# Performance work log

Hardware: AMD Instinct MI355X
Metric: run time of the kernel (lower is better)

The kernel has to match this reference:

```python
import jax, jax.numpy as jnp
import numpy as np

EMBD_DIM = 512
HIDDEN_DIM = 512
TARGET_DIM = 128
BATCH = 64
MAX_SET = 2048


def setup_inputs() -> dict:
    key = jax.random.key(0)
    ks = jax.random.split(key, 10)
    E, H, T = EMBD_DIM, HIDDEN_DIM, TARGET_DIM
    s = lambda fan_in: 1.0 / np.sqrt(fan_in)
    return {
        "words": jax.random.normal(ks[0], (BATCH, MAX_SET, E), dtype=jnp.float32),
        # attention_layer: Linear(2E -> H) followed by tanh; v: (H, 1)
        "W_att": jax.random.uniform(ks[1], (2 * E, H), jnp.float32, -s(2 * E), s(2 * E)),
        "b_att": jax.random.uniform(ks[2], (H,), jnp.float32, -s(2 * E), s(2 * E)),
        "v": jax.random.normal(ks[3], (H, 1), dtype=jnp.float32),
        # pred_net: Linear(E,H) -> ReLU -> Linear(H,H) -> ReLU -> Linear(H,T)
        "W1": jax.random.uniform(ks[4], (E, H), jnp.float32, -s(E), s(E)),
        "b1": jax.random.uniform(ks[5], (H,), jnp.float32, -s(E), s(E)),
        "W2": jax.random.uniform(ks[6], (H, H), jnp.float32, -s(H), s(H)),
        "b2": jax.random.uniform(ks[7], (H,), jnp.float32, -s(H), s(H)),
        "W3": jax.random.uniform(ks[8], (H, T), jnp.float32, -s(H), s(H)),
        "b3": jax.random.uniform(ks[9], (T,), jnp.float32, -s(H), s(H)),
    }


def reference(words, W_att, b_att, v, W1, b1, W2, b2, W3, b3):
    # words: [B, S, E]. A row is "valid" iff its feature-sum is nonzero
    # (matches words.sum(2).abs().sign() in the torch code).
    mask = jnp.sign(jnp.abs(words.sum(-1)))           # [B, S], 0/1 float
    lengths = mask.sum(axis=1, keepdims=True)          # [B, 1]
    # context = mean over valid rows (padded rows are exactly zero)
    context = words.sum(axis=1, keepdims=True) / lengths[..., None]  # [B, 1, E]
    context = jnp.broadcast_to(context, words.shape)   # [B, S, E]

    x = jnp.concatenate([words, context], axis=-1)     # [B, S, 2E]
    h = jnp.tanh(x @ W_att + b_att)                    # [B, S, H]
    scores = (h @ v)[..., 0]                           # [B, S]

    # per-segment softmax over valid rows only (masked_select + per-batch
    # Softmax in the original == masked softmax here)
    scores = jnp.where(mask > 0, scores, jnp.full_like(scores, -1e30))
    attn = jax.nn.softmax(scores, axis=1)              # [B, S]

    rep = jnp.einsum("bs,bse->be", attn, words)        # [B, E]

    pred = jax.nn.relu(rep @ W1 + b1)
    pred = jax.nn.relu(pred @ W2 + b2)
    pred = pred @ W3 + b3                              # [B, T]
    return pred
```

## Files before the change

kernel.cpp:

```cpp
#include <hip/hip_runtime.h>
#include <hip/hip_bf16.h>
#include <hip/hip_fp16.h>
#include <math.h>

#define B 64
#define S 2048
#define E 512
#define HD 512
#define TD 128
#define M_TOT (B*S)

#define OFF_MASK   0
#define OFF_CTXP   (OFF_MASK + B*S)
#define OFF_LENP   (OFF_CTXP + 8*B*E)
#define OFF_CB     (OFF_LENP + 8*B)
#define OFF_REPP   (OFF_CB + B*HD)
#define OFF_SC     (OFF_REPP + 8*B*E)
#define OFF_WPK    (OFF_SC + B*S)

typedef __attribute__((ext_vector_type(8))) short short8;
typedef __attribute__((ext_vector_type(4))) float f32x4;

__device__ inline unsigned int f2hu(float x) {
    __half h = __float2half(x);
    unsigned short u; __builtin_memcpy(&u, &h, 2); return (unsigned int)u;
}

__device__ inline float fast_tanh(float x) {
    float a = fabsf(x);
    float e = __expf(-2.0f * a);
    float r = (1.0f - e) / (1.0f + e);
    return copysignf(r, x);
}

__global__ __launch_bounds__(256)
void k0_pack(const float* __restrict__ W_att, unsigned short* __restrict__ Wpk)
{
    int tid = blockIdx.x*256 + threadIdx.x;
    int e = tid >> 9, h = tid & 511;
    float w = W_att[(size_t)e*HD + h];
    int kstep = e >> 5, kb = (e >> 3) & 3, j = e & 7, f = h >> 4, l15 = h & 15;
    size_t dst = ((((size_t)kstep*32 + f)*64) + kb*16 + l15)*8 + j;
    Wpk[dst] = (unsigned short)f2hu(w);
}

__global__ __launch_bounds__(256)
void k1_maskcol(const float* __restrict__ words, float* __restrict__ mask,
                float* __restrict__ ctxp, float* __restrict__ lenp)
{
    int bid = blockIdx.x;
    int b = bid >> 3, ch = bid & 7;
    int t = threadIdx.x;
    int w = t >> 6, l = t & 63;
    __shared__ __align__(16) float colred[4][E];
    __shared__ float lenred[4];
    const float* base = words + (size_t)(b * S + ch * 256) * E;
    float4 c0 = make_float4(0.f,0.f,0.f,0.f), c1 = make_float4(0.f,0.f,0.f,0.f);
    float wlen = 0.0f;
    for (int r = w; r < 256; r += 4) {
        const float* row = base + (size_t)r * E;
        float4 a  = *(const float4*)(row + 4*l);
        float4 bb = *(const float4*)(row + 256 + 4*l);
        float rs = a.x+a.y+a.z+a.w + bb.x+bb.y+bb.z+bb.w;
        #pragma unroll
        for (int m = 1; m < 64; m <<= 1) rs += __shfl_xor(rs, m);
        c0.x += a.x;  c0.y += a.y;  c0.z += a.z;  c0.w += a.w;
        c1.x += bb.x; c1.y += bb.y; c1.z += bb.z; c1.w += bb.w;
        if (l == 0) {
            float mv = (rs != 0.0f) ? 1.0f : 0.0f;
            mask[(size_t)b*S + ch*256 + r] = mv;
            wlen += mv;
        }
    }
    *(float4*)&colred[w][4*l]       = c0;
    *(float4*)&colred[w][256 + 4*l] = c1;
    if (l == 0) lenred[w] = wlen;
    __syncthreads();
    float s1 = colred[0][t]+colred[1][t]+colred[2][t]+colred[3][t];
    float s2 = colred[0][t+256]+colred[1][t+256]+colred[2][t+256]+colred[3][t+256];
    size_t o = ((size_t)ch * B + b) * E;
    ctxp[o + t]       = s1;
    ctxp[o + t + 256] = s2;
    if (t == 0) lenp[ch*B + b] = lenred[0]+lenred[1]+lenred[2]+lenred[3];
}

__global__ __launch_bounds__(256)
void k2_cb(const float* __restrict__ W_att, const float* __restrict__ b_att,
           const float* __restrict__ ctxp, const float* __restrict__ lenp,
           float* __restrict__ cb)
{
    int bid = blockIdx.x;
    int b = bid >> 1, hc = bid & 1;
    int t = threadIdx.x;
    __shared__ float ctxL[E];
    float len = 0.f;
    #pragma unroll
    for (int k = 0; k < 8; ++k) len += lenp[k*B + b];
    float inv = 1.0f / len;
    for (int c = t; c < E; c += 256) {
        float sv = 0.f;
        #pragma unroll
        for (int k = 0; k < 8; ++k) sv += ctxp[((size_t)k*B + b)*E + c];
        ctxL[c] = sv * inv;
    }
    __syncthreads();
    int h = hc*256 + t;
    const float* Wb = W_att + (size_t)E * HD;
    float a0 = b_att[h], a1 = 0.f, a2 = 0.f, a3 = 0.f;
    #pragma unroll 4
    for (int e = 0; e < E; e += 4) {
        a0 += ctxL[e]   * Wb[(size_t)e*HD + h];
        a1 += ctxL[e+1] * Wb[(size_t)(e+1)*HD + h];
        a2 += ctxL[e+2] * Wb[(size_t)(e+2)*HD + h];
        a3 += ctxL[e+3] * Wb[(size_t)(e+3)*HD + h];
    }
    cb[(size_t)b*HD + h] = (a0 + a1) + (a2 + a3);
}

__global__ __launch_bounds__(512, 2)
void k3_scores(const float* __restrict__ words,
               const unsigned short* __restrict__ Wpk,
               const float* __restrict__ cb, const float* __restrict__ v,
               float* __restrict__ sc)
{
    __shared__ __align__(16) unsigned char smem[16384];
    int mt = blockIdx.x;
    int m0 = mt * 128;
    int b  = m0 >> 11;
    int t = threadIdx.x;
    int lane = t & 63, wid = t >> 6;
    int wr = wid >> 2, wc = wid & 3;

    f32x4 acc[4][8];
    #pragma unroll
    for (int i = 0; i < 4; ++i)
        #pragma unroll
        for (int j = 0; j < 8; ++j) acc[i][j] = (f32x4)0.0f;

    int sF = (t >> 6) & 7, skb = (t >> 4) & 3, sl15 = t & 15;
    int srow = sF*16 + sl15;
    const float* aSrc = words + (size_t)(m0 + srow)*E + skb*8;

    const unsigned short* bBase = Wpk + (((size_t)(wc*8))*64 + lane)*8;
#define LDB(kst,cf) (*(const short8*)(bBase + ((size_t)(kst)*32 + (cf))*512))

    float4 pa0, pa1, qa0, qa1;
#define LOADA(P0, P1, s) do { const float* _s = aSrc + (s)*32; \
        P0 = *(const float4*)(_s); P1 = *(const float4*)(_s + 4); } while(0)
#define STAGEA(buf, P0, P1) do { \
        unsigned int u0 = f2hu(P0.x) | (f2hu(P0.y) << 16); \
        unsigned int u1 = f2hu(P0.z) | (f2hu(P0.w) << 16); \
        unsigned int u2 = f2hu(P1.x) | (f2hu(P1.y) << 16); \
        unsigned int u3 = f2hu(P1.z) | (f2hu(P1.w) << 16); \
        *(uint4*)&(buf)[t*16] = make_uint4(u0, u1, u2, u3); } while(0)

    unsigned char* sm0 = smem;
    unsigned char* sm1 = smem + 8192;

    short8 bA[8], bB[8];

    LOADA(pa0, pa1, 0);
    STAGEA(sm0, pa0, pa1);
    LOADA(pa0, pa1, 1);
    LOADA(qa0, qa1, 2);
    #pragma unroll
    for (int cf = 0; cf < 8; ++cf) bA[cf] = LDB(0, cf);
    __syncthreads();

#define KBODY(k, BUFC, BUFN, P0, P1, BCUR, BNEXT) do { \
        short8 ah[4]; \
        _Pragma("unroll") \
        for (int rf = 0; rf < 4; ++rf) \
            ah[rf] = *(const short8*)&(BUFC)[(wr*4 + rf)*1024 + lane*16]; \
        if ((k) < 15) { \
            _Pragma("unroll") \
            for (int cf = 0; cf < 8; ++cf) BNEXT[cf] = LDB((k)+1, cf); \
            STAGEA(BUFN, P0, P1); \
        } \
        if ((k) < 13) LOADA(P0, P1, (k) + 3); \
        _Pragma("unroll") \
        for (int cf = 0; cf < 8; ++cf) { \
            _Pragma("unroll") \
            for (int rf = 0; rf < 4; ++rf) \
                acc[rf][cf] = __builtin_amdgcn_mfma_f32_16x16x32_f16(ah[rf], BCUR[cf], acc[rf][cf], 0, 0, 0); \
        } \
        __syncthreads(); } while(0)

    KBODY( 0, sm0, sm1, pa0, pa1, bA, bB);
    KBODY( 1, sm1, sm0, qa0, qa1, bB, bA);
    KBODY( 2, sm0, sm1, pa0, pa1, bA, bB);
    KBODY( 3, sm1, sm0, qa0, qa1, bB, bA);
    KBODY( 4, sm0, sm1, pa0, pa1, bA, bB);
    KBODY( 5, sm1, sm0, qa0, qa1, bB, bA);
    KBODY( 6, sm0, sm1, pa0, pa1, bA, bB);
    KBODY( 7, sm1, sm0, qa0, qa1, bB, bA);
    KBODY( 8, sm0, sm1, pa0, pa1, bA, bB);
    KBODY( 9, sm1, sm0, qa0, qa1, bB, bA);
    KBODY(10, sm0, sm1, pa0, pa1, bA, bB);
    KBODY(11, sm1, sm0, qa0, qa1, bB, bA);
    KBODY(12, sm0, sm1, pa0, pa1, bA, bB);
    KBODY(13, sm1, sm0, qa0, qa1, bB, bA);
    KBODY(14, sm0, sm1, pa0, pa1, bA, bB);
    KBODY(15, sm1, sm0, qa0, qa1, bB, bA);
#undef KBODY
#undef LOADA
#undef STAGEA
#undef LDB

    float ssum[4][4];
    #pragma unroll
    for (int i = 0; i < 4; ++i)
        #pragma unroll
        for (int rr = 0; rr < 4; ++rr) ssum[i][rr] = 0.f;

    #pragma unroll
    for (int cf = 0; cf < 8; ++cf) {
        int col = wc*128 + cf*16 + (lane & 15);
        float cbv = cb[(size_t)b*HD + col];
        float vv  = v[col];
        #pragma unroll
        for (int rf = 0; rf < 4; ++rf)
            #pragma unroll
            for (int rr = 0; rr < 4; ++rr)
                ssum[rf][rr] += fast_tanh(acc[rf][cf][rr] + cbv) * vv;
    }
    #pragma unroll
    for (int m = 1; m < 16; m <<= 1)
        #pragma unroll
        for (int rf = 0; rf < 4; ++rf)
            #pragma unroll
            for (int rr = 0; rr < 4; ++rr)
                ssum[rf][rr] += __shfl_xor(ssum[rf][rr], m);

    float* scr = (float*)smem;
    if ((lane & 15) == 0) {
        #pragma unroll
        for (int rf = 0; rf < 4; ++rf)
            #pragma unroll
            for (int rr = 0; rr < 4; ++rr)
                scr[wc*128 + wr*64 + rf*16 + (lane >> 4)*4 + rr] = ssum[rf][rr];
    }
    __syncthreads();
    if (t < 128) {
        float val = (scr[t] + scr[128 + t]) + (scr[256 + t] + scr[384 + t]);
        sc[(size_t)m0 + t] = val;
    }
}

__global__ __launch_bounds__(256)
void k4_rep(const float* __restrict__ words, const float* __restrict__ sc,
            const float* __restrict__ mask, float* __restrict__ repp)
{
    int bid = blockIdx.x;
    int b = bid >> 3, ch = bid & 7;
    int t = threadIdx.x;
    __shared__ float red[256];
    __shared__ float wrow[256];

    float xs[8];
    float mx = -1e30f;
    #pragma unroll
    for (int k = 0; k < 8; ++k) {
        size_t m = (size_t)b*S + 256*k + t;
        float x = sc[m];
        x = (mask[m] > 0.0f) ? x : -1e30f;
        xs[k] = x; mx = fmaxf(mx, x);
    }
    red[t] = mx; __syncthreads();
    for (int off = 128; off > 0; off >>= 1) {
        if (t < off) red[t] = fmaxf(red[t], red[t+off]);
        __syncthreads();
    }
    float gmax = red[0]; __syncthreads();
    float se = 0.f;
    #pragma unroll
    for (int k = 0; k < 8; ++k) se += expf(xs[k] - gmax);
    red[t] = se; __syncthreads();
    for (int off = 128; off > 0; off >>= 1) {
        if (t < off) red[t] += red[t+off];
        __syncthreads();
    }
    float den = red[0];
    wrow[t] = expf(xs[ch] - gmax) / den;
    __syncthreads();

    const float* base = words + (size_t)(b*S + ch*256)*E + 2*t;
    float2 acc = make_float2(0.f, 0.f);
    #pragma unroll 4
    for (int rr = 0; rr < 256; ++rr) {
        float2 wv = *(const float2*)(base + (size_t)rr*E);
        float a = wrow[rr];
        acc.x = fmaf(a, wv.x, acc.x);
        acc.y = fmaf(a, wv.y, acc.y);
    }
    size_t o = ((size_t)ch*B + b)*E + 2*t;
    *(float2*)&repp[o] = acc;
}

__global__ __launch_bounds__(256)
void k5_mlp(const float* __restrict__ repp,
            const float* __restrict__ W1, const float* __restrict__ b1,
            const float* __restrict__ W2, const float* __restrict__ b2,
            const float* __restrict__ W3, const float* __restrict__ b3,
            float* __restrict__ out)
{
    int b = blockIdx.x;
    int t = threadIdx.x;
    __shared__ float xL[HD];
    __shared__ float yL[HD];
    for (int c = t; c < E; c += 256) {
        float sv = 0.f;
        #pragma unroll
        for (int k = 0; k < 8; ++k) sv += repp[((size_t)k*B + b)*E + c];
        xL[c] = sv;
    }
    __syncthreads();
    #pragma unroll
    for (int oo = 0; oo < 2; ++oo) {
        int h = oo*256 + t;
        float a0 = b1[h], a1 = 0.f, a2 = 0.f, a3 = 0.f;
        #pragma unroll 4
        for (int e = 0; e < E; e += 4) {
            a0 += xL[e]   * W1[(size_t)e*HD + h];
            a1 += xL[e+1] * W1[(size_t)(e+1)*HD + h];
            a2 += xL[e+2] * W1[(size_t)(e+2)*HD + h];
            a3 += xL[e+3] * W1[(size_t)(e+3)*HD + h];
        }
        yL[h] = fmaxf((a0 + a1) + (a2 + a3), 0.f);
    }
    __syncthreads();
    float l2v[2];
    #pragma unroll
    for (int oo = 0; oo < 2; ++oo) {
        int h = oo*256 + t;
        float a0 = b2[h], a1 = 0.f, a2 = 0.f, a3 = 0.f;
        #pragma unroll 4
        for (int e = 0; e < HD; e += 4) {
            a0 += yL[e]   * W2[(size_t)e*HD + h];
            a1 += yL[e+1] * W2[(size_t)(e+1)*HD + h];
            a2 += yL[e+2] * W2[(size_t)(e+2)*HD + h];
            a3 += yL[e+3] * W2[(size_t)(e+3)*HD + h];
        }
        l2v[oo] = fmaxf((a0 + a1) + (a2 + a3), 0.f);
    }
    __syncthreads();
    xL[t] = l2v[0]; xL[256 + t] = l2v[1];
    __syncthreads();
    if (t < TD) {
        float a0 = b3[t], a1 = 0.f, a2 = 0.f, a3 = 0.f;
        #pragma unroll 4
        for (int e = 0; e < HD; e += 4) {
            a0 += xL[e]   * W3[(size_t)e*TD + t];
            a1 += xL[e+1] * W3[(size_t)(e+1)*TD + t];
            a2 += xL[e+2] * W3[(size_t)(e+2)*TD + t];
            a3 += xL[e+3] * W3[(size_t)(e+3)*TD + t];
        }
        out[(size_t)b*TD + t] = (a0 + a1) + (a2 + a3);
    }
}

extern "C" void kernel_launch(void* const* d_in, const int* in_sizes, int n_in,
                              void* d_out, int out_size, void* d_ws, size_t ws_size,
                              hipStream_t stream)
{
    const float* words = (const float*)d_in[0];
    const float* W_att = (const float*)d_in[1];
    const float* b_att = (const float*)d_in[2];
    const float* v     = (const float*)d_in[3];
    const float* W1    = (const float*)d_in[4];
    const float* b1    = (const float*)d_in[5];
    const float* W2    = (const float*)d_in[6];
    const float* b2    = (const float*)d_in[7];
    const float* W3    = (const float*)d_in[8];
    const float* b3    = (const float*)d_in[9];
    (void)in_sizes; (void)n_in; (void)out_size; (void)ws_size;

    float* ws   = (float*)d_ws;
    float* mask = ws + OFF_MASK;
    float* ctxp = ws + OFF_CTXP;
    float* lenp = ws + OFF_LENP;
    float* cb   = ws + OFF_CB;
    float* repp = ws + OFF_REPP;
    float* sc   = ws + OFF_SC;
    unsigned short* Wpk = (unsigned short*)(ws + OFF_WPK);
    float* out  = (float*)d_out;

    hipLaunchKernelGGL(k0_pack,    dim3(1024), dim3(256), 0, stream, W_att, Wpk);
    hipLaunchKernelGGL(k1_maskcol, dim3(B*8),  dim3(256), 0, stream, words, mask, ctxp, lenp);
    hipLaunchKernelGGL(k2_cb,      dim3(B*2),  dim3(256), 0, stream, W_att, b_att, ctxp, lenp, cb);
    hipLaunchKernelGGL(k3_scores,  dim3(1024), dim3(512), 0, stream, words, Wpk, cb, v, sc);
    hipLaunchKernelGGL(k4_rep,     dim3(B*8),  dim3(256), 0, stream, words, sc, mask, repp);
    hipLaunchKernelGGL(k5_mlp,     dim3(B),    dim3(256), 0, stream, repp, W1, b1, W2, b2, W3, b3, out);
}
```

Before: 322.1 us.

## Fuse masked softmax and weighted sum into scores kernel via online-softmax partials

The scores kernel now applies the mask, computes a per-128-row chunk max and exp-sum, and accumulates the exp-weighted sum of the word rows into per-chunk partials while that tile is likely still in cache. The MLP kernel merges the 16 chunk partials per batch with a log-sum-exp rescale, which removes the separate rep kernel and its second full pass over the words tensor from global memory. In exchange the scores kernel gains an epilogue with extra barriers and a 128-row strided read per thread, and it uses __expf instead of expf.

```diff
diff --git a/kernel.cpp b/kernel.cpp
--- a/kernel.cpp
+++ b/kernel.cpp
@@ -9,14 +9,16 @@
 #define HD 512
 #define TD 128
 #define M_TOT (B*S)
+#define NCHUNK (M_TOT/128)
 
 #define OFF_MASK   0
 #define OFF_CTXP   (OFF_MASK + B*S)
 #define OFF_LENP   (OFF_CTXP + 8*B*E)
 #define OFF_CB     (OFF_LENP + 8*B)
-#define OFF_REPP   (OFF_CB + B*HD)
-#define OFF_SC     (OFF_REPP + 8*B*E)
-#define OFF_WPK    (OFF_SC + B*S)
+#define OFF_PP     (OFF_CB + B*HD)
+#define OFF_ML     (OFF_PP + NCHUNK*E)
+#define OFF_LL     (OFF_ML + NCHUNK)
+#define OFF_WPK    (OFF_LL + NCHUNK)
 
 typedef __attribute__((ext_vector_type(8))) short short8;
 typedef __attribute__((ext_vector_type(4))) float f32x4;
@@ -121,7 +123,8 @@
 void k3_scores(const float* __restrict__ words,
                const unsigned short* __restrict__ Wpk,
                const float* __restrict__ cb, const float* __restrict__ v,
-               float* __restrict__ sc)
+               const float* __restrict__ mask,
+               float* __restrict__ Pp, float* __restrict__ Ml, float* __restrict__ Ll)
 {
     __shared__ __align__(16) unsigned char smem[16384];
     int mt = blockIdx.x;
@@ -232,7 +235,12 @@
             for (int rr = 0; rr < 4; ++rr)
                 ssum[rf][rr] += __shfl_xor(ssum[rf][rr], m);
 
-    float* scr = (float*)smem;
+    float* fsm = (float*)smem;
+    float* scr   = fsm;
+    float* scm   = fsm + 512;
+    float* wrow  = fsm + 640;
+    float* redv  = fsm + 768;
+
     if ((lane & 15) == 0) {
         #pragma unroll
         for (int rf = 0; rf < 4; ++rf)
@@ -241,64 +249,43 @@
                 scr[wc*128 + wr*64 + rf*16 + (lane >> 4)*4 + rr] = ssum[rf][rr];
     }
     __syncthreads();
+
     if (t < 128) {
         float val = (scr[t] + scr[128 + t]) + (scr[256 + t] + scr[384 + t]);
-        sc[(size_t)m0 + t] = val;
-    }
+        float mk = mask[(size_t)m0 + t];
+        scm[t] = (mk > 0.0f) ? val : -1e30f;
+    }
+    __syncthreads();
+    if (t < 64) {
+        float m1 = fmaxf(scm[t], scm[t + 64]);
+        #pragma unroll
+        for (int mm = 1; mm < 64; mm <<= 1) m1 = fmaxf(m1, __shfl_xor(m1, mm));
+        if (t == 0) redv[0] = m1;
+    }
+    __syncthreads();
+    float m_c = redv[0];
+    if (t < 128) wrow[t] = __expf(scm[t] - m_c);
+    __syncthreads();
+    if (t < 64) {
+        float s1 = wrow[t] + wrow[t + 64];
+        #pragma unroll
+        for (int mm = 1; mm < 64; mm <<= 1) s1 += __shfl_xor(s1, mm);
+        if (t == 0) redv[1] = s1;
+    }
+
+    float P = 0.f;
+    const float* wbase = words + (size_t)m0*E + t;
+    #pragma unroll 8
+    for (int r2 = 0; r2 < 128; ++r2)
+        P = fmaf(wrow[r2], wbase[(size_t)r2*E], P);
+    __syncthreads();
+    Pp[(size_t)mt*E + t] = P;
+    if (t == 0) { Ml[mt] = m_c; Ll[mt] = redv[1]; }
 }
 
 __global__ __launch_bounds__(256)
-void k4_rep(const float* __restrict__ words, const float* __restrict__ sc,
-            const float* __restrict__ mask, float* __restrict__ repp)
-{
-    int bid = blockIdx.x;
-    int b = bid >> 3, ch = bid & 7;
-    int t = threadIdx.x;
-    __shared__ float red[256];
-    __shared__ float wrow[256];
-
-    float xs[8];
-    float mx = -1e30f;
-    #pragma unroll
-    for (int k = 0; k < 8; ++k) {
-        size_t m = (size_t)b*S + 256*k + t;
-        float x = sc[m];
-        x = (mask[m] > 0.0f) ? x : -1e30f;
-        xs[k] = x; mx = fmaxf(mx, x);
-    }
-    red[t] = mx; __syncthreads();
-    for (int off = 128; off > 0; off >>= 1) {
-        if (t < off) red[t] = fmaxf(red[t], red[t+off]);
-        __syncthreads();
-    }
-    float gmax = red[0]; __syncthreads();
-    float se = 0.f;
-    #pragma unroll
-    for (int k = 0; k < 8; ++k) se += expf(xs[k] - gmax);
-    red[t] = se; __syncthreads();
-    for (int off = 128; off > 0; off >>= 1) {
-        if (t < off) red[t] += red[t+off];
-        __syncthreads();
-    }
-    float den = red[0];
-    wrow[t] = expf(xs[ch] - gmax) / den;
-    __syncthreads();
-
-    const float* base = words + (size_t)(b*S + ch*256)*E + 2*t;
-    float2 acc = make_float2(0.f, 0.f);
-    #pragma unroll 4
-    for (int rr = 0; rr < 256; ++rr) {
-        float2 wv = *(const float2*)(base + (size_t)rr*E);
-        float a = wrow[rr];
-        acc.x = fmaf(a, wv.x, acc.x);
-        acc.y = fmaf(a, wv.y, acc.y);
-    }
-    size_t o = ((size_t)ch*B + b)*E + 2*t;
-    *(float2*)&repp[o] = acc;
-}
-
-__global__ __launch_bounds__(256)
-void k5_mlp(const float* __restrict__ repp,
+void k5_mlp(const float* __restrict__ Pp, const float* __restrict__ Ml,
+            const float* __restrict__ Ll,
             const float* __restrict__ W1, const float* __restrict__ b1,
             const float* __restrict__ W2, const float* __restrict__ b2,
             const float* __restrict__ W3, const float* __restrict__ b3,
@@ -308,11 +295,29 @@
     int t = threadIdx.x;
     __shared__ float xL[HD];
     __shared__ float yL[HD];
-    for (int c = t; c < E; c += 256) {
+    __shared__ float wf[16];
+
+    if (t == 0) {
+        float M = -3e38f;
+        #pragma unroll
+        for (int c = 0; c < 16; ++c) M = fmaxf(M, Ml[b*16 + c]);
+        float den = 0.f;
+        #pragma unroll
+        for (int c = 0; c < 16; ++c) den += __expf(Ml[b*16 + c] - M) * Ll[b*16 + c];
+        float inv = 1.0f / den;
+        #pragma unroll
+        for (int c = 0; c < 16; ++c) wf[c] = __expf(Ml[b*16 + c] - M) * inv;
+    }
+    __syncthreads();
+
+    #pragma unroll
+    for (int oo = 0; oo < 2; ++oo) {
+        int e = oo*256 + t;
         float sv = 0.f;
         #pragma unroll
-        for (int k = 0; k < 8; ++k) sv += repp[((size_t)k*B + b)*E + c];
-        xL[c] = sv;
+        for (int c = 0; c < 16; ++c)
+            sv += wf[c] * Pp[(size_t)(b*16 + c)*E + e];
+        xL[e] = sv;
     }
     __syncthreads();
     #pragma unroll
@@ -380,15 +385,15 @@
     float* ctxp = ws + OFF_CTXP;
     float* lenp = ws + OFF_LENP;
     float* cb   = ws + OFF_CB;
-    float* repp = ws + OFF_REPP;
-    float* sc   = ws + OFF_SC;
+    float* Pp   = ws + OFF_PP;
+    float* Ml   = ws + OFF_ML;
+    float* Ll   = ws + OFF_LL;
     unsigned short* Wpk = (unsigned short*)(ws + OFF_WPK);
     float* out  = (float*)d_out;
 
     hipLaunchKernelGGL(k0_pack,    dim3(1024), dim3(256), 0, stream, W_att, Wpk);
     hipLaunchKernelGGL(k1_maskcol, dim3(B*8),  dim3(256), 0, stream, words, mask, ctxp, lenp);
     hipLaunchKernelGGL(k2_cb,      dim3(B*2),  dim3(256), 0, stream, W_att, b_att, ctxp, lenp, cb);
-    hipLaunchKernelGGL(k3_scores,  dim3(1024), dim3(512), 0, stream, words, Wpk, cb, v, sc);
-    hipLaunchKernelGGL(k4_rep,     dim3(B*8),  dim3(256), 0, stream, words, sc, mask, repp);
-    hipLaunchKernelGGL(k5_mlp,     dim3(B),    dim3(256), 0, stream, repp, W1, b1, W2, b2, W3, b3, out);
-}
+    hipLaunchKernelGGL(k3_scores,  dim3(1024), dim3(512), 0, stream, words, Wpk, cb, v, mask, Pp, Ml, Ll);
+    hipLaunchKernelGGL(k5_mlp,     dim3(B),    dim3(256), 0, stream, Pp, Ml, Ll, W1, b1, W2, b2, W3, b3, out);
+}
```

Result: faster. 308.5 us (-4.2%).
